# Optimization experiments

Measured on AMD Instinct MI355X. Metric: run time of the kernel, lower is better.

The kernel has to match this reference:

```python
import jax, jax.numpy as jnp
import numpy as np
from math import lgamma

B = 8
RES = 64
RES_OUT = 32
L_IN = RES // 2 - 1        # 31
L_OUT = RES_OUT // 2 - 1   # 15
SPINS_IN = (0, 1)
SPINS_OUT = (0, 1, 2)
C_IN = 64
C_OUT = 128
K_IN = (L_IN + 1) ** 2     # 1024 coefficients, ordered by (ell, m): idx = ell^2 + (m + ell)
K_OUT = (L_OUT + 1) ** 2   # 256
EPS_BN = 1e-5
EPS_NL = 1e-6


def _wigner_d_col(l, s, thetas):
    """Wigner small-d column d^l_{m,-s}(theta) for m in [-l, l]; (2l+1, n_theta)."""
    n = -s
    out = np.zeros((2 * l + 1, thetas.size))
    if l < abs(s):
        return out
    cb = np.cos(thetas / 2.0)
    sb = np.sin(thetas / 2.0)
    for mi, m in enumerate(range(-l, l + 1)):
        pref = 0.5 * (lgamma(l + m + 1) + lgamma(l - m + 1)
                      + lgamma(l + n + 1) + lgamma(l - n + 1))
        acc = np.zeros_like(thetas)
        for k in range(max(0, n - m), min(l + n, l - m) + 1):
            lg = pref - (lgamma(l + n - k + 1) + lgamma(k + 1)
                         + lgamma(m - n + k + 1) + lgamma(l - m - k + 1))
            acc += ((-1.0) ** (m - n + k)) * np.exp(lg) \
                   * cb ** (2 * l + n - m - 2 * k) * sb ** (m - n + 2 * k)
        out[mi] = acc
    return out


def _sylm_grid(spin, ell_max, res):
    """Spin-weighted spherical harmonics sampled on equiangular grid: (K, res, res)."""
    thetas = (np.arange(res) + 0.5) * np.pi / res
    phis = np.arange(res) * 2.0 * np.pi / res
    Y = np.zeros(((ell_max + 1) ** 2, res, res), dtype=np.complex64)
    phase = np.exp(1j * np.outer(np.arange(-ell_max, ell_max + 1), phis))
    for l in range(ell_max + 1):
        d = _wigner_d_col(l, spin, thetas)               # (2l+1, res)
        norm = np.sqrt((2 * l + 1) / (4.0 * np.pi))
        for mi, m in enumerate(range(-l, l + 1)):
            Y[l * l + mi] = (((-1.0) ** m) * norm * d[mi][:, None]
                             * phase[m + ell_max][None, :])
    return Y


# Deterministic transform constants (computed once at import).
_THETA = (np.arange(RES) + 0.5) * np.pi / RES
_QUAD_W = (np.sin(_THETA) * (np.pi / RES) * (2.0 * np.pi / RES)).astype(np.float32)
Y_IN = np.stack([_sylm_grid(s, L_IN, RES) for s in SPINS_IN])          # (Si,K_IN,RES,RES)
Y_IN_W = (np.conj(Y_IN) * _QUAD_W[None, None, :, None]).astype(np.complex64)
Y_OUT = np.stack([_sylm_grid(s, L_OUT, RES_OUT) for s in SPINS_OUT])   # (So,K_OUT,32,32)
ELL_OUT = np.floor(np.sqrt(np.arange(K_OUT))).astype(np.int32)         # degree of each coeff


def setup_inputs() -> dict:
    key = jax.random.key(0)
    ks = jax.random.split(key, 8)
    shape_x = (B, RES, RES, len(SPINS_IN), C_IN)
    kern_shape = (L_IN + 1, len(SPINS_IN), len(SPINS_OUT), C_IN, C_OUT)
    scale = 1.0 / np.sqrt(len(SPINS_IN) * C_IN)
    return {
        "x_real": jax.random.normal(ks[0], shape_x, jnp.float32),
        "x_imag": jax.random.normal(ks[1], shape_x, jnp.float32),
        "kernel_real": jax.random.normal(ks[2], kern_shape, jnp.float32) * scale,
        "kernel_imag": jax.random.normal(ks[3], kern_shape, jnp.float32) * scale,
        "gamma": jax.random.uniform(ks[4], (len(SPINS_OUT), C_OUT), jnp.float32, 0.5, 1.5),
        "beta_real": jax.random.normal(ks[5], (len(SPINS_OUT), C_OUT), jnp.float32) * 0.1,
        "beta_imag": jax.random.normal(ks[6], (len(SPINS_OUT), C_OUT), jnp.float32) * 0.1,
        "nonlin_bias": jax.random.normal(ks[7], (len(SPINS_OUT), C_OUT), jnp.float32) * 0.1,
    }


def _forward(x_real, x_imag, kernel_real, kernel_imag, gamma,
             beta_real, beta_imag, nonlin_bias):
    x = x_real + 1j * x_imag                                   # (B,RES,RES,Si,Ci)
    # Forward spin-weighted spherical harmonic transform, per input spin.
    coeffs = jnp.einsum('btpiu,iktp->bkiu', x, jnp.asarray(Y_IN_W))  # (B,K_IN,Si,Ci)
    # Spectral pooling: keep degrees ell <= L_OUT (coeffs ordered by ell).
    coeffs = coeffs[:, :K_OUT]
    # Per-degree spectral convolution mixing spins and channels.
    kernel = (kernel_real + 1j * kernel_imag)[jnp.asarray(ELL_OUT)]  # (K_OUT,Si,So,Ci,Co)
    out_coeffs = jnp.einsum('bkiu,kisud->bksd', coeffs, kernel)      # (B,K_OUT,So,Co)
    # Inverse transform on the downsampled grid, per output spin.
    fmap = jnp.einsum('bksd,sktp->btpsd', out_coeffs, jnp.asarray(Y_OUT))
    # Equivariant batch norm: mean subtraction only for spin 0 channels.
    spin0 = (jnp.asarray(np.array(SPINS_OUT)) == 0)[:, None]         # (So,1)
    mean = jnp.mean(fmap, axis=(0, 1, 2)) * spin0                    # (So,Co)
    centered = fmap - mean
    var = jnp.mean(jnp.abs(centered) ** 2, axis=(0, 1, 2))           # (So,Co)
    beta = (beta_real + 1j * beta_imag) * spin0
    y = centered * (gamma / jnp.sqrt(var + EPS_BN)) + beta
    # Magnitude nonlinearity: y * relu(|y| + b) / (|y| + eps).
    mag = jnp.abs(y)
    return y * (jax.nn.relu(mag + nonlin_bias) / (mag + EPS_NL))


def reference(x_real, x_imag, kernel_real, kernel_imag, gamma,
              beta_real, beta_imag, nonlin_bias):
    return _forward(x_real, x_imag, kernel_real, kernel_imag, gamma,
                    beta_real, beta_imag, nonlin_bias)
```

## Files before the change

### kernel.cpp

```cpp
#include <hip/hip_runtime.h>
#include <math.h>


#define PI_D 3.14159265358979323846

#define OFF_A_IN    ((size_t)24320)
#define OFF_A_OUT   ((size_t)155648)
#define OFF_STATS   ((size_t)254208)
#define OFF_R1      ((size_t)260608)
#define OFF_R2      ((size_t)25426688)

__device__ inline int isqrt_k(int k) {
    int l = (int)sqrtf((float)k + 0.5f);
    while (l * l > k) --l;
    while ((l + 1) * (l + 1) <= k) ++l;
    return l;
}

__device__ double wigner_d_dev(int l, int m, int n, double theta, const double* lf) {
    int an = n < 0 ? -n : n;
    int am = m < 0 ? -m : m;
    if (l < an || l < am) return 0.0;
    double cb = cos(0.5 * theta), sb = sin(0.5 * theta);
    double pref = 0.5 * (lf[l + m] + lf[l - m] + lf[l + n] + lf[l - n]);
    int kmin = max(0, n - m), kmax = min(l + n, l - m);
    if (kmax < kmin) return 0.0;
    double p = pow(cb, (double)(2 * l + n - m - 2 * kmin)) * pow(sb, (double)(m - n + 2 * kmin));
    double r = (sb * sb) / (cb * cb);
    double acc = 0.0;
    for (int k = kmin; k <= kmax; ++k) {
        double lg = pref - (lf[l + n - k] + lf[k] + lf[m - n + k] + lf[l - m - k]);
        double term = exp(lg) * p;
        acc += ((m - n + k) & 1) ? -term : term;
        p *= r;
    }
    return acc;
}

__global__ __launch_bounds__(256) void k_tables(float* __restrict__ A_in,
                                                float* __restrict__ A_out,
                                                float* __restrict__ stats) {
    __shared__ double lf[40];
    if (threadIdx.x == 0) {
        lf[0] = 0.0;
        for (int j = 1; j < 40; ++j) lf[j] = lf[j - 1] + log((double)j);
    }
    __syncthreads();
    int idx = blockIdx.x * 256 + threadIdx.x;
    if (idx < 32768) {
        int t = idx & 63, k = (idx >> 6) & 255, i = idx >> 14;
        int l = isqrt_k(k);
        int m = k - l * l - l;
        int n = -i;
        double theta = ((double)t + 0.5) * PI_D / 64.0;
        double w = sin(theta) * (PI_D / 64.0) * (2.0 * PI_D / 64.0);
        double norm = sqrt((2.0 * l + 1.0) / (4.0 * PI_D));
        double d = wigner_d_dev(l, m, n, theta, lf);
        A_in[idx] = (float)(((m & 1) ? -1.0 : 1.0) * norm * w * d);
        return;
    }
    idx -= 32768;
    if (idx < 24576) {
        int t = idx & 31, k = (idx >> 5) & 255, s = idx >> 13;
        int l = isqrt_k(k);
        int m = k - l * l - l;
        int n = -s;
        double theta = ((double)t + 0.5) * PI_D / 32.0;
        double norm = sqrt((2.0 * l + 1.0) / (4.0 * PI_D));
        double d = wigner_d_dev(l, m, n, theta, lf);
        A_out[idx] = (float)(((m & 1) ? -1.0 : 1.0) * norm * d);
        return;
    }
    idx -= 24576;
    if (idx < 1152) stats[idx] = 0.f;
}

__global__ __launch_bounds__(512, 2) void k_phi_in(const float* __restrict__ xr,
                                                   const float* __restrict__ xi,
                                                   float2* __restrict__ F) {
    int bt = blockIdx.x;
    int iu = threadIdx.x & 127, mh = threadIdx.x >> 7;
    int mi0 = mh * 8;
    float2 acc[8], w[8], st[8];
#pragma unroll
    for (int j = 0; j < 8; ++j) {
        int m = mi0 + j - 15;
        float sy, sx;
        __sincosf(-(float)m * (float)(PI_D / 32.0), &sy, &sx);
        st[j] = make_float2(sx, sy);
        w[j] = make_float2(1.f, 0.f);
        acc[j] = make_float2(0.f, 0.f);
    }
    const float* xrb = xr + (size_t)bt * 8192 + iu;
    const float* xib = xi + (size_t)bt * 8192 + iu;
    for (int p = 0; p < 32; ++p) {
        float a  = xrb[(size_t)p * 128];
        float b  = xib[(size_t)p * 128];
        float a2 = xrb[(size_t)(p + 32) * 128];
        float b2 = xib[(size_t)(p + 32) * 128];
        float sar = a + a2, sai = b + b2;
        float dar = a - a2, dai = b - b2;
#pragma unroll
        for (int j = 0; j < 8; ++j) {
            float ur = (j & 1) ? sar : dar;
            float ui = (j & 1) ? sai : dai;
            acc[j].x += ur * w[j].x - ui * w[j].y;
            acc[j].y += ur * w[j].y + ui * w[j].x;
            float nx = w[j].x * st[j].x - w[j].y * st[j].y;
            w[j].y = w[j].x * st[j].y + w[j].y * st[j].x;
            w[j].x = nx;
        }
    }
    float2* Fb = F + (size_t)bt * 31 * 128 + iu;
#pragma unroll
    for (int j = 0; j < 8; ++j) {
        int mi = mi0 + j;
        if (mi < 31) Fb[(size_t)mi * 128] = acc[j];
    }
}

__global__ __launch_bounds__(512, 2) void k_theta_in(const float2* __restrict__ F,
                                                     const float* __restrict__ A_in,
                                                     float2* __restrict__ coeffs) {
    __shared__ float A[2][16][64];
    __shared__ float2 red[2][16][128];
    int mi = blockIdx.x, b = blockIdx.y;
    int m = mi - 15;
    int am = m < 0 ? -m : m;
    int tid = threadIdx.x;
    for (int idx = tid; idx < 2048; idx += 512) {
        int i = idx >> 10, j = (idx >> 6) & 15, t = idx & 63;
        float v = 0.f;
        if (j >= am) v = A_in[((size_t)i * 256 + (j * j + j + m)) * 64 + t];
        A[i][j][t] = v;
    }
    __syncthreads();
    int iu = tid & 127, th = tid >> 7, i = iu >> 6;
    float2 acc[16];
#pragma unroll
    for (int j = 0; j < 16; ++j) acc[j] = make_float2(0.f, 0.f);
    const float2* Fb = F + ((size_t)b * 64 * 31 + mi) * 128 + iu;
    for (int tt = 0; tt < 16; ++tt) {
        int t = th * 16 + tt;
        float2 f = Fb[(size_t)t * 31 * 128];
#pragma unroll
        for (int j = 0; j < 16; ++j) {
            float a = A[i][j][t];
            acc[j].x += a * f.x;
            acc[j].y += a * f.y;
        }
    }
    if (th >= 2) {
#pragma unroll
        for (int j = 0; j < 16; ++j) red[th - 2][j][iu] = acc[j];
    }
    __syncthreads();
    if (th < 2) {
#pragma unroll
        for (int j = 0; j < 16; ++j) {
            float2 r = red[th][j][iu];
            acc[j].x += r.x;
            acc[j].y += r.y;
        }
    }
    __syncthreads();
    if (th == 1) {
#pragma unroll
        for (int j = 0; j < 16; ++j) red[0][j][iu] = acc[j];
    }
    __syncthreads();
    if (th == 0) {
#pragma unroll
        for (int j = 0; j < 16; ++j) {
            if (j >= am) {
                float2 r = red[0][j][iu];
                coeffs[((size_t)b * 256 + (j * j + j + m)) * 128 + iu] =
                    make_float2(acc[j].x + r.x, acc[j].y + r.y);
            }
        }
    }
}

__global__ __launch_bounds__(384, 3) void k_mix(const float2* __restrict__ coeffs,
                                                const float* __restrict__ kr,
                                                const float* __restrict__ ki,
                                                float2* __restrict__ oc) {
    __shared__ float2 cs[2][2][128];
    int k0 = blockIdx.x * 2;
    int b0 = blockIdx.y * 2;
    int tid = threadIdx.x;
    for (int idx = tid; idx < 512; idx += 384) {
        int kk = idx >> 8, bb = (idx >> 7) & 1, iu = idx & 127;
        cs[kk][bb][iu] = coeffs[((size_t)(b0 + bb) * 256 + (k0 + kk)) * 128 + iu];
    }
    __syncthreads();
    int kk = tid / 192, r = tid % 192;
    int s = r >> 6, dp = r & 63;
    int k = k0 + kk;
    int l = isqrt_k(k);
    float2 acc[2][2];
#pragma unroll
    for (int bb = 0; bb < 2; ++bb) {
        acc[bb][0] = make_float2(0.f, 0.f);
        acc[bb][1] = make_float2(0.f, 0.f);
    }
    for (int i = 0; i < 2; ++i) {
        const float2* krp = (const float2*)(kr + (size_t)(6 * l + 3 * i + s) * 8192) + dp;
        const float2* kip = (const float2*)(ki + (size_t)(6 * l + 3 * i + s) * 8192) + dp;
        float2 w0[4], w1[4];
#pragma unroll
        for (int j = 0; j < 4; ++j) { w0[j] = krp[(size_t)j * 64]; w1[j] = kip[(size_t)j * 64]; }
        for (int ub = 0; ub < 64; ub += 4) {
            float2 n0[4], n1[4];
            if (ub + 4 < 64) {
#pragma unroll
                for (int j = 0; j < 4; ++j) {
                    n0[j] = krp[(size_t)(ub + 4 + j) * 64];
                    n1[j] = kip[(size_t)(ub + 4 + j) * 64];
                }
            }
#pragma unroll
            for (int j = 0; j < 4; ++j) {
                int iu = i * 64 + ub + j;
                float2 wr = w0[j], wi = w1[j];
#pragma unroll
                for (int bb = 0; bb < 2; ++bb) {
                    float2 cv = cs[kk][bb][iu];
                    acc[bb][0].x += cv.x * wr.x - cv.y * wi.x;
                    acc[bb][0].y += cv.x * wi.x + cv.y * wr.x;
                    acc[bb][1].x += cv.x * wr.y - cv.y * wi.y;
                    acc[bb][1].y += cv.x * wi.y + cv.y * wr.y;
                }
            }
#pragma unroll
            for (int j = 0; j < 4; ++j) { w0[j] = n0[j]; w1[j] = n1[j]; }
        }
    }
#pragma unroll
    for (int bb = 0; bb < 2; ++bb) {
        float4 stv = make_float4(acc[bb][0].x, acc[bb][0].y, acc[bb][1].x, acc[bb][1].y);
        *(float4*)&oc[((size_t)(b0 + bb) * 256 + k) * 384 + s * 128 + 2 * dp] = stv;
    }
}

__global__ __launch_bounds__(384, 2) void k_theta_out(const float2* __restrict__ oc,
                                                      const float* __restrict__ A_out,
                                                      float2* __restrict__ G,
                                                      float* __restrict__ ssr,
                                                      float* __restrict__ ssi,
                                                      float* __restrict__ ssq) {
    __shared__ float Ao[3][16][32];
    int mi = blockIdx.x, b = blockIdx.y;
    int m = mi - 15;
    int am = m < 0 ? -m : m;
    int tid = threadIdx.x;
    for (int idx = tid; idx < 1536; idx += 384) {
        int s = idx >> 9, j = (idx >> 5) & 15, t = idx & 31;
        float v = 0.f;
        if (j >= am) v = A_out[((size_t)s * 256 + (j * j + j + m)) * 32 + t];
        Ao[s][j][t] = v;
    }
    __syncthreads();
    int s = tid >> 7;
    float2 c[16];
#pragma unroll
    for (int j = 0; j < 16; ++j) {
        c[j] = make_float2(0.f, 0.f);
        if (j >= am) c[j] = oc[((size_t)b * 256 + (j * j + j + m)) * 384 + tid];
    }
    float sq = 0.f, sr = 0.f, si = 0.f;
    for (int t = 0; t < 32; ++t) {
        float fr = 0.f, fi = 0.f;
#pragma unroll
        for (int j = 0; j < 16; ++j) {
            float a = Ao[s][j][t];
            fr += a * c[j].x;
            fi += a * c[j].y;
        }
        G[(((size_t)b * 32 + t) * 31 + mi) * 384 + tid] = make_float2(fr, fi);
        sq += fr * fr + fi * fi;
        if (mi == 15) { sr += fr; si += fi; }
    }
    atomicAdd(&ssq[tid], sq);
    if (mi == 15) {
        atomicAdd(&ssr[tid], sr);
        atomicAdd(&ssi[tid], si);
    }
}

__global__ __launch_bounds__(384, 1) void k_synth_final(const float2* __restrict__ G,
                                                        const float* __restrict__ ssr,
                                                        const float* __restrict__ ssi,
                                                        const float* __restrict__ ssq,
                                                        const float* __restrict__ gamma,
                                                        const float* __restrict__ betar,
                                                        const float* __restrict__ betai,
                                                        const float* __restrict__ bias,
                                                        float* __restrict__ out) {
    int bt = blockIdx.x;
    int sd = threadIdx.x, s = sd >> 7;
    float2 g[31], st[31];
#pragma unroll
    for (int mi = 0; mi < 31; ++mi) {
        g[mi] = G[((size_t)bt * 31 + mi) * 384 + sd];
        float sy, sx;
        __sincosf((float)(mi - 15) * (float)(PI_D / 16.0), &sy, &sx);
        st[mi] = make_float2(sx, sy);
    }
    const float invN = 1.0f / 256.0f;
    float mur = 0.f, mui = 0.f;
    if (s == 0) { mur = ssr[sd] * invN; mui = ssi[sd] * invN; }
    float var = ssq[sd] * invN - (mur * mur + mui * mui);
    float scale = gamma[sd] / sqrtf(var + 1e-5f);
    float br = (s == 0) ? betar[sd] : 0.f;
    float bi = (s == 0) ? betai[sd] : 0.f;
    float bb = bias[sd];
    float* ob = out + (size_t)bt * 32 * 384 + sd;
    for (int p = 0; p < 16; ++p) {
        float fr = 0.f, fi = 0.f, fr2 = 0.f, fi2 = 0.f;
#pragma unroll
        for (int mi = 0; mi < 31; ++mi) {
            fr += g[mi].x;
            fi += g[mi].y;
            if (mi & 1) { fr2 += g[mi].x; fi2 += g[mi].y; }
            else        { fr2 -= g[mi].x; fi2 -= g[mi].y; }
        }
        {
            float yr = (fr - mur) * scale + br;
            float yi = (fi - mui) * scale + bi;
            float mag = sqrtf(yr * yr + yi * yi);
            float f = fmaxf(mag + bb, 0.f) / (mag + 1e-6f);
            ob[(size_t)p * 384] = yr * f;
        }
        {
            float yr = (fr2 - mur) * scale + br;
            float yi = (fi2 - mui) * scale + bi;
            float mag = sqrtf(yr * yr + yi * yi);
            float f = fmaxf(mag + bb, 0.f) / (mag + 1e-6f);
            ob[(size_t)(p + 16) * 384] = yr * f;
        }
#pragma unroll
        for (int mi = 0; mi < 31; ++mi) {
            float nx = g[mi].x * st[mi].x - g[mi].y * st[mi].y;
            g[mi].y = g[mi].x * st[mi].y + g[mi].y * st[mi].x;
            g[mi].x = nx;
        }
    }
}

extern "C" void kernel_launch(void* const* d_in, const int* in_sizes, int n_in,
                              void* d_out, int out_size, void* d_ws, size_t ws_size,
                              hipStream_t stream) {
    const float* xr    = (const float*)d_in[0];
    const float* xi    = (const float*)d_in[1];
    const float* kr    = (const float*)d_in[2];
    const float* ki    = (const float*)d_in[3];
    const float* gamma = (const float*)d_in[4];
    const float* betar = (const float*)d_in[5];
    const float* betai = (const float*)d_in[6];
    const float* bias  = (const float*)d_in[7];
    float* out = (float*)d_out;

    char* ws = (char*)d_ws;
    float*  A_in   = (float*)(ws + OFF_A_IN);
    float*  A_out  = (float*)(ws + OFF_A_OUT);
    float*  stats  = (float*)(ws + OFF_STATS);
    float*  ssr    = stats;
    float*  ssi    = stats + 384;
    float*  ssq    = stats + 768;
    float2* F      = (float2*)(ws + OFF_R1);
    float2* oc     = (float2*)(ws + OFF_R1);
    float2* coeffs = (float2*)(ws + OFF_R2);
    float2* G      = (float2*)(ws + OFF_R2);

    k_tables<<<229, 256, 0, stream>>>(A_in, A_out, stats);
    k_phi_in<<<512, 512, 0, stream>>>(xr, xi, F);
    k_theta_in<<<dim3(31, 8), 512, 0, stream>>>(F, A_in, coeffs);
    k_mix<<<dim3(128, 4), 384, 0, stream>>>(coeffs, kr, ki, oc);
    k_theta_out<<<dim3(31, 8), 384, 0, stream>>>(oc, A_out, G, ssr, ssi, ssq);
    k_synth_final<<<256, 384, 0, stream>>>(G, ssr, ssi, ssq,
                                           gamma, betar, betai, bias, out);
}
```

Measured before the change: 194.7 us.

## Fuse table generation into phi kernel and use recurrence for Wigner-d

Merges the table-building kernel into the phi-transform kernel as extra blocks, removing one launch and letting table generation overlap with the phi FFT work. The Wigner-d evaluation now computes only the first term with exp/log and gets later terms by a ratio recurrence, replacing per-term exp and pow calls in double precision. Log-factorials move to a constant array instead of a serial shared-memory build. The recurrence can change rounding slightly compared with direct summation.

```diff
diff --git a/kernel.cpp b/kernel.cpp
--- a/kernel.cpp
+++ b/kernel.cpp
@@ -10,6 +10,18 @@
 #define OFF_R1      ((size_t)260608)
 #define OFF_R2      ((size_t)25426688)
 
+__constant__ double LF[31] = {
+    0.0, 0.0, 0.6931471805599453, 1.791759469228055, 3.1780538303479458,
+    4.787491742782046, 6.579251212010101, 8.525161361065415,
+    10.604602902745251, 12.801827480081469, 15.104412573075516,
+    17.502307845873887, 19.987214495661885, 22.552163853123425,
+    25.19122118273868, 27.89927138384089, 30.671860106080672,
+    33.50507345013689, 36.39544520803305, 39.339884187199495,
+    42.335616460753485, 45.38013889847691, 48.47118135183523,
+    51.60667556776438, 54.78472939811232, 58.00360522298052,
+    61.261701761002, 64.55753862700634, 67.88974313718154,
+    71.25703896716801, 74.65823634883016};
+
 __device__ inline int isqrt_k(int k) {
     int l = (int)sqrtf((float)k + 0.5f);
     while (l * l > k) --l;
@@ -17,67 +29,64 @@
     return l;
 }
 
-__device__ double wigner_d_dev(int l, int m, int n, double theta, const double* lf) {
+__device__ double wigner_d_rec(int l, int m, int n, double theta) {
     int an = n < 0 ? -n : n;
     int am = m < 0 ? -m : m;
     if (l < an || l < am) return 0.0;
-    double cb = cos(0.5 * theta), sb = sin(0.5 * theta);
-    double pref = 0.5 * (lf[l + m] + lf[l - m] + lf[l + n] + lf[l - n]);
     int kmin = max(0, n - m), kmax = min(l + n, l - m);
     if (kmax < kmin) return 0.0;
-    double p = pow(cb, (double)(2 * l + n - m - 2 * kmin)) * pow(sb, (double)(m - n + 2 * kmin));
+    double cb = cos(0.5 * theta), sb = sin(0.5 * theta);
+    double pref = 0.5 * (LF[l + m] + LF[l - m] + LF[l + n] + LF[l - n]);
+    double lterm = pref
+        - (LF[l + n - kmin] + LF[kmin] + LF[m - n + kmin] + LF[l - m - kmin])
+        + (double)(2 * l + n - m - 2 * kmin) * log(cb)
+        + (double)(m - n + 2 * kmin) * log(sb);
+    double term = exp(lterm);
+    if ((m - n + kmin) & 1) term = -term;
     double r = (sb * sb) / (cb * cb);
-    double acc = 0.0;
-    for (int k = kmin; k <= kmax; ++k) {
-        double lg = pref - (lf[l + n - k] + lf[k] + lf[m - n + k] + lf[l - m - k]);
-        double term = exp(lg) * p;
-        acc += ((m - n + k) & 1) ? -term : term;
-        p *= r;
+    double acc = term;
+    for (int k = kmin; k < kmax; ++k) {
+        term *= -((double)((l + n - k) * (l - m - k)) * r)
+                / ((double)((k + 1) * (m - n + k + 1)));
+        acc += term;
     }
     return acc;
 }
 
-__global__ __launch_bounds__(256) void k_tables(float* __restrict__ A_in,
-                                                float* __restrict__ A_out,
-                                                float* __restrict__ stats) {
-    __shared__ double lf[40];
-    if (threadIdx.x == 0) {
-        lf[0] = 0.0;
-        for (int j = 1; j < 40; ++j) lf[j] = lf[j - 1] + log((double)j);
-    }
-    __syncthreads();
-    int idx = blockIdx.x * 256 + threadIdx.x;
-    if (idx < 32768) {
-        int t = idx & 63, k = (idx >> 6) & 255, i = idx >> 14;
-        int l = isqrt_k(k);
-        int m = k - l * l - l;
-        int n = -i;
-        double theta = ((double)t + 0.5) * PI_D / 64.0;
-        double w = sin(theta) * (PI_D / 64.0) * (2.0 * PI_D / 64.0);
-        double norm = sqrt((2.0 * l + 1.0) / (4.0 * PI_D));
-        double d = wigner_d_dev(l, m, n, theta, lf);
-        A_in[idx] = (float)(((m & 1) ? -1.0 : 1.0) * norm * w * d);
+__global__ __launch_bounds__(512, 2) void k_phi_tables(const float* __restrict__ xr,
+                                                       const float* __restrict__ xi,
+                                                       float2* __restrict__ F,
+                                                       float* __restrict__ A_in,
+                                                       float* __restrict__ A_out,
+                                                       float* __restrict__ stats) {
+    if (blockIdx.x >= 512) {
+        int idx = (blockIdx.x - 512) * 512 + threadIdx.x;
+        if (idx < 32768) {
+            int t = idx & 63, k = (idx >> 6) & 255, i = idx >> 14;
+            int l = isqrt_k(k);
+            int m = k - l * l - l;
+            double theta = ((double)t + 0.5) * PI_D / 64.0;
+            double w = sin(theta) * (PI_D / 64.0) * (2.0 * PI_D / 64.0);
+            double norm = sqrt((2.0 * l + 1.0) / (4.0 * PI_D));
+            double d = wigner_d_rec(l, m, -i, theta);
+            A_in[idx] = (float)(((m & 1) ? -1.0 : 1.0) * norm * w * d);
+            return;
+        }
+        idx -= 32768;
+        if (idx < 24576) {
+            int t = idx & 31, k = (idx >> 5) & 255, s = idx >> 13;
+            int l = isqrt_k(k);
+            int m = k - l * l - l;
+            double theta = ((double)t + 0.5) * PI_D / 32.0;
+            double norm = sqrt((2.0 * l + 1.0) / (4.0 * PI_D));
+            double d = wigner_d_rec(l, m, -s, theta);
+            A_out[idx] = (float)(((m & 1) ? -1.0 : 1.0) * norm * d);
+            return;
+        }
+        idx -= 24576;
+        if (idx < 1152) stats[idx] = 0.f;
         return;
     }
-    idx -= 32768;
-    if (idx < 24576) {
-        int t = idx & 31, k = (idx >> 5) & 255, s = idx >> 13;
-        int l = isqrt_k(k);
-        int m = k - l * l - l;
-        int n = -s;
-        double theta = ((double)t + 0.5) * PI_D / 32.0;
-        double norm = sqrt((2.0 * l + 1.0) / (4.0 * PI_D));
-        double d = wigner_d_dev(l, m, n, theta, lf);
-        A_out[idx] = (float)(((m & 1) ? -1.0 : 1.0) * norm * d);
-        return;
-    }
-    idx -= 24576;
-    if (idx < 1152) stats[idx] = 0.f;
-}
-
-__global__ __launch_bounds__(512, 2) void k_phi_in(const float* __restrict__ xr,
-                                                   const float* __restrict__ xi,
-                                                   float2* __restrict__ F) {
     int bt = blockIdx.x;
     int iu = threadIdx.x & 127, mh = threadIdx.x >> 7;
     int mi0 = mh * 8;
@@ -373,8 +382,7 @@
     float2* coeffs = (float2*)(ws + OFF_R2);
     float2* G      = (float2*)(ws + OFF_R2);
 
-    k_tables<<<229, 256, 0, stream>>>(A_in, A_out, stats);
-    k_phi_in<<<512, 512, 0, stream>>>(xr, xi, F);
+    k_phi_tables<<<627, 512, 0, stream>>>(xr, xi, F, A_in, A_out, stats);
     k_theta_in<<<dim3(31, 8), 512, 0, stream>>>(F, A_in, coeffs);
     k_mix<<<dim3(128, 4), 384, 0, stream>>>(coeffs, kr, ki, oc);
     k_theta_out<<<dim3(31, 8), 384, 0, stream>>>(oc, A_out, G, ssr, ssi, ssq);
```

Measured after the change: 184.4 us. 5.3% less time.
